# Performance work log

Hardware: AMD Instinct MI355X
Metric: run time of the kernel (lower is better)

## Reference

```python
import jax, jax.numpy as jnp
import numpy as np

N_NODES = 50000
VOCAB = 2048
HID = 256
N_EDGES = 1600000


def setup_inputs() -> dict:
    key = jax.random.key(0)
    ks = jax.random.split(key, 7)
    context = jax.random.normal(ks[0], (N_NODES, VOCAB), dtype=jnp.float32)
    adj_row = jax.random.randint(ks[1], (N_EDGES,), 0, N_NODES, dtype=jnp.int64)
    adj_col = jax.random.randint(ks[2], (N_EDGES,), 0, N_NODES, dtype=jnp.int64)
    adj_val = jax.random.uniform(ks[3], (N_EDGES,), dtype=jnp.float32)
    # learned params
    context_weight = jax.random.normal(ks[4], (HID, VOCAB), dtype=jnp.float32) * 0.02
    out_w = jax.random.normal(ks[5], (VOCAB, HID), dtype=jnp.float32) * 0.02
    out_b = jnp.zeros((VOCAB,), dtype=jnp.float32)
    return {
        "context": context,
        "adj_row": adj_row,
        "adj_col": adj_col,
        "adj_val": adj_val,
        "context_weight": context_weight,
        "out_w": out_w,
        "out_b": out_b,
    }


def reference(context, adj_row, adj_col, adj_val, context_weight, out_w, out_b):
    # support = context @ context_weight.T : [N, hid]
    support = jnp.einsum('nv,hv->nh', context, context_weight)
    # spmm: out[r] += val * support[c]  (COO sparse-dense matmul)
    gathered = support[adj_col] * adj_val[:, None]          # [E, hid]
    agg = jax.ops.segment_sum(gathered, adj_row, num_segments=N_NODES)  # [N, hid]
    score = jax.nn.relu(agg)
    # out linear: hid -> vocab
    output = jnp.einsum('nh,vh->nv', score, out_w) + out_b  # [N, vocab]
    return output
```

## Files before the change

kernel.cpp:

```cpp
#include <hip/hip_runtime.h>
#include <hip/hip_bf16.h>

#define N_NODES 50000
#define VOCAB   2048
#define HID     256
#define N_EDGES 1600000

typedef __attribute__((ext_vector_type(8))) __bf16 bf16x8;
typedef __attribute__((ext_vector_type(4))) __bf16 bf16x4;
typedef __attribute__((ext_vector_type(4))) float  f32x4;

__device__ __forceinline__ void gl_lds16(const void* g, void* l) {
    __builtin_amdgcn_global_load_lds(
        (const __attribute__((address_space(1))) void*)g,
        (__attribute__((address_space(3))) void*)l, 16, 0, 0);
}

#define HIST_NB 256
#define CVT_NB  512
__global__ __launch_bounds__(256) void phase1(
    const int*   __restrict__ arow, int* __restrict__ cnt, int E,
    const float* __restrict__ w1, __bf16* __restrict__ w1b,
    const float* __restrict__ w2, __bf16* __restrict__ w2b)
{
    const int tid = threadIdx.x;
    int bid = blockIdx.x;
    if (bid < HIST_NB) {
        const int stride = HIST_NB * 256;
        for (int e4 = bid * 256 + tid; e4 < E / 4; e4 += stride) {
            const int4 r = ((const int4*)arow)[e4];
            atomicAdd(&cnt[r.x], 1); atomicAdd(&cnt[r.y], 1);
            atomicAdd(&cnt[r.z], 1); atomicAdd(&cnt[r.w], 1);
        }
        return;
    }
    bid -= HIST_NB;
    const float* w  = (bid < CVT_NB) ? w1 : w2;
    __bf16*      wb = (bid < CVT_NB) ? w1b : w2b;
    if (bid >= CVT_NB) bid -= CVT_NB;
    const int t = bid * 256 + tid;
    const float4 v = ((const float4*)w)[t];
    bf16x4 p = { (__bf16)v.x, (__bf16)v.y, (__bf16)v.z, (__bf16)v.w };
    ((bf16x4*)wb)[t] = p;
}

#define SCAN_NB 49

__global__ __launch_bounds__(256) void scan1(
    const int* __restrict__ cnt, int* __restrict__ bsum, int n)
{
    __shared__ int red[256];
    const int base = blockIdx.x * 1024 + threadIdx.x * 4;
    int s = 0;
    #pragma unroll
    for (int i = 0; i < 4; ++i) { const int idx = base + i; if (idx < n) s += cnt[idx]; }
    red[threadIdx.x] = s;
    __syncthreads();
    for (int off = 128; off > 0; off >>= 1) {
        if (threadIdx.x < off) red[threadIdx.x] += red[threadIdx.x + off];
        __syncthreads();
    }
    if (threadIdx.x == 0) bsum[blockIdx.x] = red[0];
}

__global__ __launch_bounds__(64) void scan2(int* __restrict__ bsum, int nb)
{
    if (threadIdx.x == 0) {
        int run = 0;
        for (int b = 0; b < nb; ++b) { const int v = bsum[b]; bsum[b] = run; run += v; }
        bsum[nb] = run;
    }
}

__global__ __launch_bounds__(256) void scan3(
    const int* __restrict__ cnt, const int* __restrict__ bsum,
    int* __restrict__ ptr, int* __restrict__ cursor, int n)
{
    __shared__ int hs[256];
    const int base = blockIdx.x * 1024 + threadIdx.x * 4;
    int loc[4]; int s = 0;
    #pragma unroll
    for (int i = 0; i < 4; ++i) {
        const int idx = base + i;
        loc[i] = (idx < n) ? cnt[idx] : 0;
        s += loc[i];
    }
    hs[threadIdx.x] = s;
    __syncthreads();
    for (int off = 1; off < 256; off <<= 1) {
        int v = (threadIdx.x >= off) ? hs[threadIdx.x - off] : 0;
        __syncthreads();
        hs[threadIdx.x] += v;
        __syncthreads();
    }
    int run = bsum[blockIdx.x] + ((threadIdx.x == 0) ? 0 : hs[threadIdx.x - 1]);
    #pragma unroll
    for (int i = 0; i < 4; ++i) {
        const int idx = base + i;
        if (idx < n) { ptr[idx] = run; cursor[idx] = run; }
        run += loc[i];
    }
    if (blockIdx.x == SCAN_NB - 1 && threadIdx.x == 255) ptr[n] = run;
}

#define FILL_NB 256
__global__ __launch_bounds__(256) void fill_gemm1(
    const int*    __restrict__ arow,
    const int*    __restrict__ acol,
    const float*  __restrict__ aval,
    int*          __restrict__ cursor,
    int2*         __restrict__ cpair,
    int E,
    const float*  __restrict__ Af,
    const __bf16* __restrict__ Bb,
    __bf16*       __restrict__ Cb,
    int M)
{
    constexpr int K = 2048, N = 256, BM = 64, BK = 32, nkt = K / BK;
    __shared__ float  sAf[2][BM * BK];
    __shared__ __bf16 sB [2][N  * BK];

    const int tid = threadIdx.x;
    int bid = blockIdx.x;

    if (bid < FILL_NB) {
        const int stride = FILL_NB * 256;
        for (int e4 = bid * 256 + tid; e4 < E / 4; e4 += stride) {
            const int4   r = ((const int4*)arow)[e4];
            const int4   c = ((const int4*)acol)[e4];
            const float4 v = ((const float4*)aval)[e4];
            int p;
            p = atomicAdd(&cursor[r.x], 1); cpair[p] = make_int2(c.x, __float_as_int(v.x));
            p = atomicAdd(&cursor[r.y], 1); cpair[p] = make_int2(c.y, __float_as_int(v.y));
            p = atomicAdd(&cursor[r.z], 1); cpair[p] = make_int2(c.z, __float_as_int(v.z));
            p = atomicAdd(&cursor[r.w], 1); cpair[p] = make_int2(c.w, __float_as_int(v.w));
        }
        return;
    }
    bid -= FILL_NB;

    const int lane = tid & 63;
    const int wn   = tid >> 6;
    const int half = lane >> 4;
    const int r16  = lane & 15;
    const int m0   = bid * BM;

    f32x4 acc[4][4] = {};

    auto stage = [&](int kt, int b) {
        const int k0 = kt * BK;
        #pragma unroll
        for (int i = 0; i < 2; ++i) {
            const int s   = i * 256 + tid;
            const int row = s >> 3, c = s & 7;
            const int csw = c ^ (row & 7);
            int gr = m0 + row; if (gr >= M) gr = M - 1;
            gl_lds16(&Af[(size_t)gr * K + k0 + csw * 4], &sAf[b][s * 4]);
        }
        #pragma unroll
        for (int i = 0; i < 4; ++i) {
            const int s   = i * 256 + tid;
            const int row = s >> 2, c = s & 3;
            const int csw = c ^ (row & 3);
            gl_lds16(&Bb[(size_t)row * K + k0 + csw * 8], &sB[b][s * 8]);
        }
    };
    auto step = [&](int b) {
        bf16x8 bfr[4];
        #pragma unroll
        for (int n = 0; n < 4; ++n) {
            const int brow = wn * 64 + n * 16 + r16;
            bfr[n] = *(const bf16x8*)&sB[b][brow * 32 + (half ^ (brow & 3)) * 8];
        }
        #pragma unroll
        for (int m = 0; m < 4; ++m) {
            const int arw = m * 16 + r16;
            const int rx  = arw & 7;
            const f32x4 lo = *(const f32x4*)&sAf[b][arw * 32 + ((2 * half)     ^ rx) * 4];
            const f32x4 hi = *(const f32x4*)&sAf[b][arw * 32 + ((2 * half + 1) ^ rx) * 4];
            const bf16x8 af = { (__bf16)lo.x, (__bf16)lo.y, (__bf16)lo.z, (__bf16)lo.w,
                                (__bf16)hi.x, (__bf16)hi.y, (__bf16)hi.z, (__bf16)hi.w };
            #pragma unroll
            for (int n = 0; n < 4; ++n)
                acc[m][n] = __builtin_amdgcn_mfma_f32_16x16x32_bf16(
                                af, bfr[n], acc[m][n], 0, 0, 0);
        }
    };

    stage(0, 0);
    __syncthreads();
    for (int kt = 0; kt < nkt; ++kt) {
        const int cur = kt & 1;
        if (kt + 1 < nkt) stage(kt + 1, cur ^ 1);
        step(cur);
        __syncthreads();
    }

    #pragma unroll
    for (int m = 0; m < 4; ++m) {
        #pragma unroll
        for (int j = 0; j < 4; ++j) {
            const int gr = m0 + m * 16 + half * 4 + j;
            if (gr >= M) continue;
            #pragma unroll
            for (int n = 0; n < 4; ++n) {
                const int gc = wn * 64 + n * 16 + r16;
                Cb[(size_t)gr * N + gc] = (__bf16)acc[m][n][j];
            }
        }
    }
}

__global__ __launch_bounds__(256) void spmm_gather(
    const int*    __restrict__ ptr,
    const int2*   __restrict__ cpair,
    const __bf16* __restrict__ support,
    __bf16*       __restrict__ agg,
    int n)
{
    const int tid  = threadIdx.x;
    const int lane = tid & 63;
    const int row  = blockIdx.x * 4 + (tid >> 6);
    if (row >= n) return;
    const int l32 = lane & 31, ep = lane >> 5;
    const int beg = ptr[row], end = ptr[row + 1];

    float a[8] = {0.f, 0.f, 0.f, 0.f, 0.f, 0.f, 0.f, 0.f};

    auto fma8 = [&](float v, const uint4& s) {
        a[0] += v * __uint_as_float(s.x << 16);
        a[1] += v * __uint_as_float(s.x & 0xFFFF0000u);
        a[2] += v * __uint_as_float(s.y << 16);
        a[3] += v * __uint_as_float(s.y & 0xFFFF0000u);
        a[4] += v * __uint_as_float(s.z << 16);
        a[5] += v * __uint_as_float(s.z & 0xFFFF0000u);
        a[6] += v * __uint_as_float(s.w << 16);
        a[7] += v * __uint_as_float(s.w & 0xFFFF0000u);
    };

    int i = beg;
    for (; i + 8 <= end; i += 8) {
        const int2 p0 = cpair[i + ep];
        const int2 p1 = cpair[i + 2 + ep];
        const int2 p2 = cpair[i + 4 + ep];
        const int2 p3 = cpair[i + 6 + ep];
        const uint4 s0 = *(const uint4*)&support[(size_t)p0.x * HID + l32 * 8];
        const uint4 s1 = *(const uint4*)&support[(size_t)p1.x * HID + l32 * 8];
        const uint4 s2 = *(const uint4*)&support[(size_t)p2.x * HID + l32 * 8];
        const uint4 s3 = *(const uint4*)&support[(size_t)p3.x * HID + l32 * 8];
        fma8(__int_as_float(p0.y), s0);
        fma8(__int_as_float(p1.y), s1);
        fma8(__int_as_float(p2.y), s2);
        fma8(__int_as_float(p3.y), s3);
    }
    for (; i + 2 <= end; i += 2) {
        const int2 p = cpair[i + ep];
        const uint4 s = *(const uint4*)&support[(size_t)p.x * HID + l32 * 8];
        fma8(__int_as_float(p.y), s);
    }
    if (i < end && ep == 0) {
        const int2 p = cpair[i];
        const uint4 s = *(const uint4*)&support[(size_t)p.x * HID + l32 * 8];
        fma8(__int_as_float(p.y), s);
    }

    #pragma unroll
    for (int k = 0; k < 8; ++k) a[k] += __shfl_xor(a[k], 32);

    if (ep == 0) {
        bf16x8 o = { (__bf16)fmaxf(a[0], 0.f), (__bf16)fmaxf(a[1], 0.f),
                     (__bf16)fmaxf(a[2], 0.f), (__bf16)fmaxf(a[3], 0.f),
                     (__bf16)fmaxf(a[4], 0.f), (__bf16)fmaxf(a[5], 0.f),
                     (__bf16)fmaxf(a[6], 0.f), (__bf16)fmaxf(a[7], 0.f) };
        *(bf16x8*)&agg[(size_t)row * HID + l32 * 8] = o;
    }
}

__global__ __launch_bounds__(256) void gemm2(
    const __bf16* __restrict__ Ab,
    const __bf16* __restrict__ Bb,
    const float*  __restrict__ bias,
    float*        __restrict__ C,
    int M)
{
    constexpr int K = 256, N = 2048, BM = 128, BN = 128, BK = 32;
    constexpr int NBY = N / BN, nkt = K / BK;
    __shared__ __bf16 sA[3][BM * BK];
    __shared__ __bf16 sB[3][BN * BK];

    const int tid  = threadIdx.x;
    const int lane = tid & 63;
    const int wid  = tid >> 6;
    const int wm   = wid >> 1;
    const int wn   = wid & 1;
    const int half = lane >> 4;
    const int r16  = lane & 15;

    const int nwg = gridDim.x, cpx = nwg >> 3;
    const int wg  = (blockIdx.x & 7) * cpx + (blockIdx.x >> 3);
    const int m0  = (wg / NBY) * BM;
    const int n0  = (wg % NBY) * BN;

    f32x4 acc[4][4] = {};

    auto stage = [&](int kt, int b) {
        const int k0 = kt * BK;
        #pragma unroll
        for (int i = 0; i < 2; ++i) {
            const int s   = i * 256 + tid;
            const int row = s >> 2, c = s & 3;
            const int csw = c ^ (row & 3);
            int gr = m0 + row; if (gr >= M) gr = M - 1;
            gl_lds16(&Ab[(size_t)gr * K + k0 + csw * 8], &sA[b][s * 8]);
        }
        #pragma unroll
        for (int i = 0; i < 2; ++i) {
            const int s   = i * 256 + tid;
            const int row = s >> 2, c = s & 3;
            const int csw = c ^ (row & 3);
            gl_lds16(&Bb[(size_t)(n0 + row) * K + k0 + csw * 8], &sB[b][s * 8]);
        }
    };
    auto step = [&](int b) {
        bf16x8 bfr[4];
        #pragma unroll
        for (int n = 0; n < 4; ++n) {
            const int brow = wn * 64 + n * 16 + r16;
            bfr[n] = *(const bf16x8*)&sB[b][brow * 32 + (half ^ (brow & 3)) * 8];
        }
        #pragma unroll
        for (int m = 0; m < 4; ++m) {
            const int arw = wm * 64 + m * 16 + r16;
            const bf16x8 af = *(const bf16x8*)&sA[b][arw * 32 + (half ^ (arw & 3)) * 8];
            #pragma unroll
            for (int n = 0; n < 4; ++n)
                acc[m][n] = __builtin_amdgcn_mfma_f32_16x16x32_bf16(
                                af, bfr[n], acc[m][n], 0, 0, 0);
        }
    };

    stage(0, 0);
    stage(1, 1);
    for (int t = 0; t < nkt; ++t) {
        if (t + 1 < nkt) asm volatile("s_waitcnt vmcnt(4)" ::: "memory");
        else             asm volatile("s_waitcnt vmcnt(0)" ::: "memory");
        __builtin_amdgcn_s_barrier();
        __builtin_amdgcn_sched_barrier(0);
        step(t % 3);
        if (t + 2 < nkt) stage(t + 2, (t + 2) % 3);
    }

    #pragma unroll
    for (int m = 0; m < 4; ++m) {
        #pragma unroll
        for (int j = 0; j < 4; ++j) {
            const int gr = m0 + wm * 64 + m * 16 + half * 4 + j;
            if (gr >= M) continue;
            #pragma unroll
            for (int n = 0; n < 4; ++n) {
                const int gc = n0 + wn * 64 + n * 16 + r16;
                __builtin_nontemporal_store(acc[m][n][j] + bias[gc],
                                            &C[(size_t)gr * N + gc]);
            }
        }
    }
}

extern "C" void kernel_launch(void* const* d_in, const int* in_sizes, int n_in,
                              void* d_out, int out_size, void* d_ws, size_t ws_size,
                              hipStream_t stream) {
    const float* context  = (const float*)d_in[0];
    const int*   adj_row  = (const int*)  d_in[1];
    const int*   adj_col  = (const int*)  d_in[2];
    const float* adj_val  = (const float*)d_in[3];
    const float* ctx_w    = (const float*)d_in[4];
    const float* out_w    = (const float*)d_in[5];
    const float* out_b    = (const float*)d_in[6];
    float*       out      = (float*)d_out;

    char* ws = (char*)d_ws;
    __bf16* support_b = (__bf16*)ws;  ws += (size_t)N_NODES * HID * 2;
    __bf16* agg_b     = (__bf16*)ws;  ws += (size_t)N_NODES * HID * 2;
    __bf16* ctxw_b    = (__bf16*)ws;  ws += (size_t)HID * VOCAB * 2;
    __bf16* outw_b    = (__bf16*)ws;  ws += (size_t)VOCAB * HID * 2;
    int*    csr_ptr   = (int*)ws;     ws += ((size_t)N_NODES + 16) * 4;
    int*    cnt       = (int*)ws;     ws += (size_t)N_NODES * 4;
    int*    cursor    = (int*)ws;     ws += (size_t)N_NODES * 4;
    int*    bsum      = (int*)ws;     ws += ((size_t)SCAN_NB + 16) * 4;
    int2*   cpair     = (int2*)ws;    ws += (size_t)N_EDGES * 8;

    hipMemsetAsync(cnt, 0, (size_t)N_NODES * 4, stream);

    phase1<<<dim3(HIST_NB + 2 * CVT_NB), 256, 0, stream>>>(
        adj_row, cnt, N_EDGES, ctx_w, ctxw_b, out_w, outw_b);

    scan1<<<SCAN_NB, 256, 0, stream>>>(cnt, bsum, N_NODES);
    scan2<<<1, 64, 0, stream>>>(bsum, SCAN_NB);
    scan3<<<SCAN_NB, 256, 0, stream>>>(cnt, bsum, csr_ptr, cursor, N_NODES);

    fill_gemm1<<<dim3(FILL_NB + (N_NODES + 63) / 64), 256, 0, stream>>>(
        adj_row, adj_col, adj_val, cursor, cpair, N_EDGES,
        context, ctxw_b, support_b, N_NODES);

    spmm_gather<<<(N_NODES + 3) / 4, 256, 0, stream>>>(
        csr_ptr, cpair, support_b, agg_b, N_NODES);

    gemm2<<<dim3(((N_NODES + 127) / 128) * (VOCAB / 128)), 256, 0, stream>>>(
        agg_b, outw_b, out_b, out, N_NODES);
}
```

Before: 541.7 us.

## Pre-pack context into swizzled bf16 tiles before first GEMM

Adds a pre-pass in phase1 that converts the fp32 context matrix to bf16 and stores it in a k-tile-major, XOR-swizzled layout padded to M_PAD rows. A new first-GEMM kernel then streams A with direct global-to-LDS 16-byte loads and uses BK=64, in place of reading fp32 and converting inside the GEMM. The aim is to halve A bytes read by the MFMA loop and simplify its staging. The cost is an extra full pass that reads 400MB of context and writes 200MB of packed data, plus more workspace, and the whole path depends on the workspace being large enough.

Result: slower. 595.6 us (+9.9%).

```diff
diff --git a/kernel.cpp b/kernel.cpp
--- a/kernel.cpp
+++ b/kernel.cpp
@@ -5,6 +5,7 @@
 #define VOCAB   2048
 #define HID     256
 #define N_EDGES 1600000
+#define M_PAD   50048
 
 typedef __attribute__((ext_vector_type(8))) __bf16 bf16x8;
 typedef __attribute__((ext_vector_type(4))) __bf16 bf16x4;
@@ -18,10 +19,13 @@
 
 #define HIST_NB 256
 #define CVT_NB  512
+#define PACK_NB 782
 __global__ __launch_bounds__(256) void phase1(
     const int*   __restrict__ arow, int* __restrict__ cnt, int E,
     const float* __restrict__ w1, __bf16* __restrict__ w1b,
-    const float* __restrict__ w2, __bf16* __restrict__ w2b)
+    const float* __restrict__ w2, __bf16* __restrict__ w2b,
+    const float* __restrict__ ctx, __bf16* __restrict__ packedA,
+    int nPack, int M)
 {
     const int tid = threadIdx.x;
     int bid = blockIdx.x;
@@ -35,14 +39,34 @@
         return;
     }
     bid -= HIST_NB;
-    const float* w  = (bid < CVT_NB) ? w1 : w2;
-    __bf16*      wb = (bid < CVT_NB) ? w1b : w2b;
-    if (bid >= CVT_NB) bid -= CVT_NB;
-    const int t = bid * 256 + tid;
-    const float4 v = ((const float4*)w)[t];
-    bf16x4 p = { (__bf16)v.x, (__bf16)v.y, (__bf16)v.z, (__bf16)v.w };
-    ((bf16x4*)wb)[t] = p;
-}
+    if (bid < 2 * CVT_NB) {
+        const float* w  = (bid < CVT_NB) ? w1 : w2;
+        __bf16*      wb = (bid < CVT_NB) ? w1b : w2b;
+        if (bid >= CVT_NB) bid -= CVT_NB;
+        const int t = bid * 256 + tid;
+        const float4 v = ((const float4*)w)[t];
+        bf16x4 p = { (__bf16)v.x, (__bf16)v.y, (__bf16)v.z, (__bf16)v.w };
+        ((bf16x4*)wb)[t] = p;
+        return;
+    }
+    bid -= 2 * CVT_NB;
+    if (bid >= nPack) return;
+    const int m0 = bid * 64;
+    #pragma unroll 4
+    for (int i = 0; i < 128; ++i) {
+        const int s   = i * 256 + tid;
+        const int row = s >> 9;
+        const int c   = s & 511;
+        int gm = m0 + row; if (gm >= M) gm = M - 1;
+        const float4 v = *(const float4*)&ctx[(size_t)gm * VOCAB + c * 4];
+        const int kt = c >> 4;
+        const int u  = (c & 15) >> 1;
+        const int us = u ^ (row & 7);
+        bf16x4 p = { (__bf16)v.x, (__bf16)v.y, (__bf16)v.z, (__bf16)v.w };
+        *(bf16x4*)&packedA[((size_t)kt * M_PAD + m0 + row) * 64 + us * 8 + (c & 1) * 4] = p;
+    }
+}
+
 
 #define SCAN_NB 49
 
@@ -104,7 +128,111 @@
 }
 
 #define FILL_NB 256
-__global__ __launch_bounds__(256) void fill_gemm1(
+__global__ __launch_bounds__(256) void fill_gemm1_packed(
+    const int*    __restrict__ arow,
+    const int*    __restrict__ acol,
+    const float*  __restrict__ aval,
+    int*          __restrict__ cursor,
+    int2*         __restrict__ cpair,
+    int E,
+    const __bf16* __restrict__ pA,
+    const __bf16* __restrict__ Bb,
+    __bf16*       __restrict__ Cb,
+    int M)
+{
+    constexpr int K = 2048, N = 256, BM = 64, BK = 64, nkt = K / BK;
+    __shared__ __bf16 sA[2][BM * BK];
+    __shared__ __bf16 sB[2][N  * BK];
+
+    const int tid = threadIdx.x;
+    int bid = blockIdx.x;
+
+    if (bid < FILL_NB) {
+        const int stride = FILL_NB * 256;
+        for (int e4 = bid * 256 + tid; e4 < E / 4; e4 += stride) {
+            const int4   r = ((const int4*)arow)[e4];
+            const int4   c = ((const int4*)acol)[e4];
+            const float4 v = ((const float4*)aval)[e4];
+            int p;
+            p = atomicAdd(&cursor[r.x], 1); cpair[p] = make_int2(c.x, __float_as_int(v.x));
+            p = atomicAdd(&cursor[r.y], 1); cpair[p] = make_int2(c.y, __float_as_int(v.y));
+            p = atomicAdd(&cursor[r.z], 1); cpair[p] = make_int2(c.z, __float_as_int(v.z));
+            p = atomicAdd(&cursor[r.w], 1); cpair[p] = make_int2(c.w, __float_as_int(v.w));
+        }
+        return;
+    }
+    bid -= FILL_NB;
+
+    const int lane = tid & 63;
+    const int wn   = tid >> 6;
+    const int half = lane >> 4;
+    const int r16  = lane & 15;
+    const int m0   = bid * BM;
+
+    f32x4 acc[4][4] = {};
+
+    auto stage = [&](int kt, int b) {
+        const __bf16* src = &pA[((size_t)kt * M_PAD + m0) * 64];
+        #pragma unroll
+        for (int i = 0; i < 2; ++i) {
+            const int s = i * 256 + tid;
+            gl_lds16(&src[s * 8], &sA[b][s * 8]);
+        }
+        #pragma unroll
+        for (int i = 0; i < 8; ++i) {
+            const int s   = i * 256 + tid;
+            const int row = s >> 3, c = s & 7;
+            const int csw = c ^ (row & 7);
+            gl_lds16(&Bb[(size_t)row * K + kt * BK + csw * 8], &sB[b][s * 8]);
+        }
+    };
+    auto step = [&](int b) {
+        #pragma unroll
+        for (int kk = 0; kk < 2; ++kk) {
+            const int q = kk * 4 + half;
+            bf16x8 bfr[4];
+            #pragma unroll
+            for (int n = 0; n < 4; ++n) {
+                const int brow = wn * 64 + n * 16 + r16;
+                bfr[n] = *(const bf16x8*)&sB[b][brow * 64 + (q ^ (brow & 7)) * 8];
+            }
+            #pragma unroll
+            for (int m = 0; m < 4; ++m) {
+                const int arw = m * 16 + r16;
+                const bf16x8 af = *(const bf16x8*)&sA[b][arw * 64 + (q ^ (arw & 7)) * 8];
+                #pragma unroll
+                for (int n = 0; n < 4; ++n)
+                    acc[m][n] = __builtin_amdgcn_mfma_f32_16x16x32_bf16(
+                                    af, bfr[n], acc[m][n], 0, 0, 0);
+            }
+        }
+    };
+
+    stage(0, 0);
+    __syncthreads();
+    for (int kt = 0; kt < nkt; ++kt) {
+        const int cur = kt & 1;
+        if (kt + 1 < nkt) stage(kt + 1, cur ^ 1);
+        step(cur);
+        __syncthreads();
+    }
+
+    #pragma unroll
+    for (int m = 0; m < 4; ++m) {
+        #pragma unroll
+        for (int j = 0; j < 4; ++j) {
+            const int gr = m0 + m * 16 + half * 4 + j;
+            if (gr >= M) continue;
+            #pragma unroll
+            for (int n = 0; n < 4; ++n) {
+                const int gc = wn * 64 + n * 16 + r16;
+                Cb[(size_t)gr * N + gc] = (__bf16)acc[m][n][j];
+            }
+        }
+    }
+}
+
+__global__ __launch_bounds__(256) void fill_gemm1_f32(
     const int*    __restrict__ arow,
     const int*    __restrict__ acol,
     const float*  __restrict__ aval,
@@ -378,7 +506,8 @@
     const float* out_b    = (const float*)d_in[6];
     float*       out      = (float*)d_out;
 
-    char* ws = (char*)d_ws;
+    char* ws0 = (char*)d_ws;
+    char* ws  = ws0;
     __bf16* support_b = (__bf16*)ws;  ws += (size_t)N_NODES * HID * 2;
     __bf16* agg_b     = (__bf16*)ws;  ws += (size_t)N_NODES * HID * 2;
     __bf16* ctxw_b    = (__bf16*)ws;  ws += (size_t)HID * VOCAB * 2;
@@ -386,21 +515,30 @@
     int*    csr_ptr   = (int*)ws;     ws += ((size_t)N_NODES + 16) * 4;
     int*    cnt       = (int*)ws;     ws += (size_t)N_NODES * 4;
     int*    cursor    = (int*)ws;     ws += (size_t)N_NODES * 4;
-    int*    bsum      = (int*)ws;     ws += ((size_t)SCAN_NB + 16) * 4;
+    int*    bsum      = (int*)ws;     ws += 320;
     int2*   cpair     = (int2*)ws;    ws += (size_t)N_EDGES * 8;
+    __bf16* packedA   = (__bf16*)ws;  ws += (size_t)M_PAD * VOCAB * 2;
+    const bool usePack = ((size_t)(ws - ws0) <= ws_size);
 
     hipMemsetAsync(cnt, 0, (size_t)N_NODES * 4, stream);
 
-    phase1<<<dim3(HIST_NB + 2 * CVT_NB), 256, 0, stream>>>(
-        adj_row, cnt, N_EDGES, ctx_w, ctxw_b, out_w, outw_b);
+    const int nPack = usePack ? PACK_NB : 0;
+    phase1<<<dim3(HIST_NB + 2 * CVT_NB + nPack), 256, 0, stream>>>(
+        adj_row, cnt, N_EDGES, ctx_w, ctxw_b, out_w, outw_b,
+        context, packedA, nPack, N_NODES);
 
     scan1<<<SCAN_NB, 256, 0, stream>>>(cnt, bsum, N_NODES);
     scan2<<<1, 64, 0, stream>>>(bsum, SCAN_NB);
     scan3<<<SCAN_NB, 256, 0, stream>>>(cnt, bsum, csr_ptr, cursor, N_NODES);
 
-    fill_gemm1<<<dim3(FILL_NB + (N_NODES + 63) / 64), 256, 0, stream>>>(
-        adj_row, adj_col, adj_val, cursor, cpair, N_EDGES,
-        context, ctxw_b, support_b, N_NODES);
+    if (usePack)
+        fill_gemm1_packed<<<dim3(FILL_NB + PACK_NB), 256, 0, stream>>>(
+            adj_row, adj_col, adj_val, cursor, cpair, N_EDGES,
+            packedA, ctxw_b, support_b, N_NODES);
+    else
+        fill_gemm1_f32<<<dim3(FILL_NB + PACK_NB), 256, 0, stream>>>(
+            adj_row, adj_col, adj_val, cursor, cpair, N_EDGES,
+            context, ctxw_b, support_b, N_NODES);
 
     spmm_gather<<<(N_NODES + 3) / 4, 256, 0, stream>>>(
         csr_ptr, cpair, support_b, agg_b, N_NODES);
```
